# Kernel optimization log

Hardware: AMD Instinct MI355X
Metric: run time of the kernel (lower is better)

Reference implementation:

```python
import jax, jax.numpy as jnp
import numpy as np


def log_g(x):
    # log of g(x) = relu(x)+0.5 for x>=0, sigmoid(x) for x<0 (continuous minGRU activation)
    return jnp.where(x >= 0, jnp.log(jax.nn.relu(x) + 0.5), -jax.nn.softplus(-x))


def parallel_scan_log(log_coeffs, log_values):
    # log_coeffs: [B,T,H], log_values: [B,T+1,H]
    a_star = jnp.pad(jnp.cumsum(log_coeffs, axis=1), ((0, 0), (1, 0), (0, 0)))  # [B,T+1,H]
    log_h = a_star + jax.lax.cumlogsumexp(log_values - a_star, axis=1)
    return jnp.exp(log_h)  # [B,T+1,H]


def setup_inputs() -> dict:
    key = jax.random.key(0)
    B, T, D, H = 8, 4096, 1024, 1024
    k1, k2, k3, k4, k5, k6 = jax.random.split(key, 6)
    scale = 1.0 / np.sqrt(D)
    return {
        "x": jax.random.normal(k1, (B, T, D), dtype=jnp.float32),
        "h_0": jax.random.uniform(k2, (B, 1, H), dtype=jnp.float32),
        "W_z": jax.random.uniform(k3, (H, D), minval=-scale, maxval=scale, dtype=jnp.float32),
        "b_z": jax.random.uniform(k4, (H,), minval=-scale, maxval=scale, dtype=jnp.float32),
        "W_h": jax.random.uniform(k5, (H, D), minval=-scale, maxval=scale, dtype=jnp.float32),
        "b_h": jax.random.uniform(k6, (H,), minval=-scale, maxval=scale, dtype=jnp.float32),
    }


def reference(x, h_0, W_z, b_z, W_h, b_h):
    # k = linear_z(x)
    k = jnp.einsum('btd,hd->bth', x, W_z) + b_z                 # [B,T,H]
    log_z = -jax.nn.softplus(-k)                                # log sigmoid(k)
    log_coeffs = -jax.nn.softplus(k)                            # log (1 - sigmoid(k))
    log_h_0 = log_g(h_0)                                        # [B,1,H]
    log_tilde_h = log_g(jnp.einsum('btd,hd->bth', x, W_h) + b_h)  # [B,T,H]
    log_values = jnp.concatenate([log_h_0, log_z + log_tilde_h], axis=1)  # [B,T+1,H]
    h = parallel_scan_log(log_coeffs, log_values)               # [B,T+1,H]
    return h
```

## Files before the change

### kernel.cpp

```cpp
#include <hip/hip_runtime.h>
#include <stdint.h>

#define B_ 8
#define T_ 4096
#define D_ 1024
#define H_ 1024
#define M_ (B_*T_)
#define K_ D_
#define N_ H_
#define TC 64
#define NC (T_/TC)

typedef short short8 __attribute__((ext_vector_type(8)));
typedef float f32x4 __attribute__((ext_vector_type(4)));
typedef unsigned short ushort8v __attribute__((ext_vector_type(8)));

__device__ __forceinline__ float bf2f(unsigned short u) {
    union { unsigned int i; float f; } x; x.i = ((unsigned int)u) << 16; return x.f;
}
__device__ __forceinline__ unsigned short f2bf(float f) {
    union { float f; unsigned int i; } x; x.f = f;
    unsigned int u = x.i;
    unsigned int r = u + 0x7fffu + ((u >> 16) & 1u);
    return (unsigned short)(r >> 16);
}
__device__ __forceinline__ void gld_lds16(const unsigned short* g, unsigned short* l) {
    __builtin_amdgcn_global_load_lds(
        (const __attribute__((address_space(1))) void*)(const void*)g,
        (__attribute__((address_space(3))) void*)(void*)l, 16, 0, 0);
}
__device__ __forceinline__ float gfun(float x) {
    return x >= 0.f ? x + 0.5f : 1.f / (1.f + __expf(-x));
}

__global__ void cvt_kernel(const float* __restrict__ src, unsigned short* __restrict__ dst, int n4) {
    int i = blockIdx.x * blockDim.x + threadIdx.x;
    const int stride = gridDim.x * blockDim.x;
    for (; i < n4; i += stride) {
        float4 v = ((const float4*)src)[i];
        ushort4 o;
        o.x = f2bf(v.x); o.y = f2bf(v.y); o.z = f2bf(v.z); o.w = f2bf(v.w);
        ((ushort4*)dst)[i] = o;
    }
}

__global__ __launch_bounds__(256) void gemm_kernel(
    const unsigned short* __restrict__ Xb,
    const unsigned short* __restrict__ Wzb,
    const unsigned short* __restrict__ Whb,
    const float* __restrict__ bz, const float* __restrict__ bh,
    unsigned short* __restrict__ KzOut, unsigned short* __restrict__ KhOut)
{
    __shared__ __align__(16) unsigned short lds_a[128 * 32];
    __shared__ __align__(16) unsigned short lds_b[128 * 32];

    const int bm = blockIdx.x;
    const int bn = blockIdx.y;
    const int mat = blockIdx.z;
    const unsigned short* Wb = mat ? Whb : Wzb;
    const float* bias = mat ? bh : bz;
    unsigned short* Out = mat ? KhOut : KzOut;

    const int tid = threadIdx.x;
    const int w = tid >> 6, lane = tid & 63;
    const int wm = w >> 1, wn = w & 1;

    f32x4 acc[4][4];
#pragma unroll
    for (int i = 0; i < 4; i++)
#pragma unroll
        for (int j = 0; j < 4; j++) acc[i][j] = (f32x4){0.f, 0.f, 0.f, 0.f};

    const int kcs = ((lane & 3) ^ ((lane >> 3) & 3)) * 8;
    const int r0 = (w * 2 + 0) * 16 + (lane >> 2);
    const int r1 = (w * 2 + 1) * 16 + (lane >> 2);
    const unsigned short* gA0 = Xb + (size_t)(bm * 128 + r0) * K_ + kcs;
    const unsigned short* gA1 = Xb + (size_t)(bm * 128 + r1) * K_ + kcs;
    const unsigned short* gB0 = Wb + (size_t)(bn * 128 + r0) * K_ + kcs;
    const unsigned short* gB1 = Wb + (size_t)(bn * 128 + r1) * K_ + kcs;
    unsigned short* la0 = &lds_a[(w * 2 + 0) * 512];
    unsigned short* la1 = &lds_a[(w * 2 + 1) * 512];
    unsigned short* lb0 = &lds_b[(w * 2 + 0) * 512];
    unsigned short* lb1 = &lds_b[(w * 2 + 1) * 512];

    const int sw = ((lane >> 4) ^ ((lane >> 1) & 3)) * 8;
    const unsigned short* ra = &lds_a[(wm * 64 + (lane & 15)) * 32 + sw];
    const unsigned short* rb = &lds_b[(wn * 64 + (lane & 15)) * 32 + sw];

    for (int k0 = 0; k0 < K_; k0 += 32) {
        __syncthreads();
        gld_lds16(gA0 + k0, la0);
        gld_lds16(gA1 + k0, la1);
        gld_lds16(gB0 + k0, lb0);
        gld_lds16(gB1 + k0, lb1);
        __syncthreads();

        short8 af[4], bfr[4];
#pragma unroll
        for (int im = 0; im < 4; im++) af[im] = *(const short8*)(ra + im * 16 * 32);
#pragma unroll
        for (int in = 0; in < 4; in++) bfr[in] = *(const short8*)(rb + in * 16 * 32);
#pragma unroll
        for (int im = 0; im < 4; im++)
#pragma unroll
            for (int in = 0; in < 4; in++)
                acc[im][in] = __builtin_amdgcn_mfma_f32_16x16x32_bf16(af[im], bfr[in], acc[im][in], 0, 0, 0);
    }

#pragma unroll
    for (int in = 0; in < 4; in++) {
        const int n = bn * 128 + wn * 64 + in * 16 + (lane & 15);
        const float bb = bias[n];
#pragma unroll
        for (int im = 0; im < 4; im++) {
            const int mq = bm * 32 + wm * 16 + im * 4 + (lane >> 4);
            ushort4 o;
            o.x = f2bf(acc[im][in][0] + bb);
            o.y = f2bf(acc[im][in][1] + bb);
            o.z = f2bf(acc[im][in][2] + bb);
            o.w = f2bf(acc[im][in][3] + bb);
            *(ushort4*)(Out + ((size_t)mq * N_ + n) * 4) = o;
        }
    }
}


__global__ __launch_bounds__(256) void scanA_kernel(const unsigned short* __restrict__ Kz,
                                                    const unsigned short* __restrict__ Kh,
                                                    float* __restrict__ Fc, float* __restrict__ Vc)
{
    const int c = blockIdx.x, b = blockIdx.y;
    const int hb = threadIdx.x * 4;
    float F[4] = {1.f, 1.f, 1.f, 1.f}, V[4] = {0.f, 0.f, 0.f, 0.f};
    size_t base = ((size_t)(b * 1024 + c * (TC / 4)) * N_ + hb) * 4;
    for (int q = 0; q < TC / 4; q++) {
        ushort8v z0 = *(const ushort8v*)(Kz + base);
        ushort8v z1 = *(const ushort8v*)(Kz + base + 8);
        ushort8v h0v = *(const ushort8v*)(Kh + base);
        ushort8v h1v = *(const ushort8v*)(Kh + base + 8);
        base += (size_t)N_ * 4;
#pragma unroll
        for (int r = 0; r < 4; r++) {
            float kzf[4] = {bf2f(z0[r]), bf2f(z0[4 + r]), bf2f(z1[r]), bf2f(z1[4 + r])};
            float khf[4] = {bf2f(h0v[r]), bf2f(h0v[4 + r]), bf2f(h1v[r]), bf2f(h1v[4 + r])};
#pragma unroll
            for (int j = 0; j < 4; j++) {
                float f = 1.f / (1.f + __expf(kzf[j]));
                float v = (1.f - f) * gfun(khf[j]);
                V[j] = f * V[j] + v;
                F[j] *= f;
            }
        }
    }
    size_t o = ((size_t)(b * NC + c)) * H_ + hb;
    *(float4*)(Fc + o) = make_float4(F[0], F[1], F[2], F[3]);
    *(float4*)(Vc + o) = make_float4(V[0], V[1], V[2], V[3]);
}

__global__ __launch_bounds__(256) void scanB_kernel(const float* __restrict__ h0,
                                                    const float* __restrict__ Fc,
                                                    const float* __restrict__ Vc,
                                                    float* __restrict__ Carry,
                                                    float* __restrict__ Out)
{
    const int b = blockIdx.x;
    const int h = threadIdx.x * 4;
    float cy[4];
#pragma unroll
    for (int j = 0; j < 4; j++) cy[j] = gfun(h0[(size_t)b * H_ + h + j]);
    *(float4*)(Out + (size_t)b * (T_ + 1) * H_ + h) = make_float4(cy[0], cy[1], cy[2], cy[3]);
    for (int c = 0; c < NC; c++) {
        size_t o = ((size_t)(b * NC + c)) * H_ + h;
        *(float4*)(Carry + o) = make_float4(cy[0], cy[1], cy[2], cy[3]);
        float4 F4 = *(const float4*)(Fc + o);
        float4 V4 = *(const float4*)(Vc + o);
        cy[0] = F4.x * cy[0] + V4.x;
        cy[1] = F4.y * cy[1] + V4.y;
        cy[2] = F4.z * cy[2] + V4.z;
        cy[3] = F4.w * cy[3] + V4.w;
    }
}

__global__ __launch_bounds__(256) void scanC_kernel(const unsigned short* __restrict__ Kz,
                                                    const unsigned short* __restrict__ Kh,
                                                    const float* __restrict__ Carry,
                                                    float* __restrict__ Out)
{
    const int c = blockIdx.x, b = blockIdx.y;
    const int hb = threadIdx.x * 4;
    float cy[4];
    {
        float4 c4 = *(const float4*)(Carry + ((size_t)(b * NC + c)) * H_ + hb);
        cy[0] = c4.x; cy[1] = c4.y; cy[2] = c4.z; cy[3] = c4.w;
    }
    size_t base = ((size_t)(b * 1024 + c * (TC / 4)) * N_ + hb) * 4;
    size_t ob = ((size_t)(b * (T_ + 1) + c * TC + 1)) * H_ + hb;
    for (int q = 0; q < TC / 4; q++) {
        ushort8v z0 = *(const ushort8v*)(Kz + base);
        ushort8v z1 = *(const ushort8v*)(Kz + base + 8);
        ushort8v h0v = *(const ushort8v*)(Kh + base);
        ushort8v h1v = *(const ushort8v*)(Kh + base + 8);
        base += (size_t)N_ * 4;
#pragma unroll
        for (int r = 0; r < 4; r++) {
            float kzf[4] = {bf2f(z0[r]), bf2f(z0[4 + r]), bf2f(z1[r]), bf2f(z1[4 + r])};
            float khf[4] = {bf2f(h0v[r]), bf2f(h0v[4 + r]), bf2f(h1v[r]), bf2f(h1v[4 + r])};
#pragma unroll
            for (int j = 0; j < 4; j++) {
                float f = 1.f / (1.f + __expf(kzf[j]));
                float v = (1.f - f) * gfun(khf[j]);
                cy[j] = f * cy[j] + v;
            }
            *(float4*)(Out + ob) = make_float4(cy[0], cy[1], cy[2], cy[3]);
            ob += H_;
        }
    }
}

extern "C" void kernel_launch(void* const* d_in, const int* in_sizes, int n_in,
                              void* d_out, int out_size, void* d_ws, size_t ws_size,
                              hipStream_t stream)
{
    const float* x  = (const float*)d_in[0];
    const float* h0 = (const float*)d_in[1];
    const float* Wz = (const float*)d_in[2];
    const float* bz = (const float*)d_in[3];
    const float* Wh = (const float*)d_in[4];
    const float* bh = (const float*)d_in[5];
    float* out = (float*)d_out;

    char* ws = (char*)d_ws;
    unsigned short* xb  = (unsigned short*)ws; ws += (size_t)M_ * K_ * 2;
    unsigned short* wzb = (unsigned short*)ws; ws += (size_t)N_ * K_ * 2;
    unsigned short* whb = (unsigned short*)ws; ws += (size_t)N_ * K_ * 2;
    unsigned short* kz  = (unsigned short*)ws; ws += (size_t)M_ * N_ * 2;
    unsigned short* kh  = (unsigned short*)ws; ws += (size_t)M_ * N_ * 2;
    float* Fc    = (float*)ws; ws += (size_t)B_ * NC * H_ * 4;
    float* Vc    = (float*)ws; ws += (size_t)B_ * NC * H_ * 4;
    float* Carry = (float*)ws; ws += (size_t)B_ * NC * H_ * 4;

    cvt_kernel<<<2048, 256, 0, stream>>>(x, xb, M_ * K_ / 4);
    cvt_kernel<<<256, 256, 0, stream>>>(Wz, wzb, N_ * K_ / 4);
    cvt_kernel<<<256, 256, 0, stream>>>(Wh, whb, N_ * K_ / 4);

    dim3 gg(M_ / 128, N_ / 128, 2);
    gemm_kernel<<<gg, 256, 0, stream>>>(xb, wzb, whb, bz, bh, kz, kh);

    scanA_kernel<<<dim3(NC, B_), 256, 0, stream>>>(kz, kh, Fc, Vc);
    scanB_kernel<<<B_, 256, 0, stream>>>(h0, Fc, Vc, Carry, out);
    scanC_kernel<<<dim3(NC, B_), 256, 0, stream>>>(kz, kh, Carry, out);
}
```

Measured before the change: 506.3 us.

## Merge conversion launches, swizzle GEMM block order, and halve scan chunk size

Combines the three fp32-to-bf16 conversion launches into one kernel that dispatches on block index, removing two launch overheads. Remaps the GEMM grid to a 1D linear index grouped so that 8 M-tiles share all N-tiles and both weight matrices, improving L2 reuse of X rows. Halves the scan chunk length so the chunked scan passes launch twice as many blocks for more parallelism, at the cost of a longer sequential carry pass in scanB and more chunk-summary traffic.

```diff
diff --git a/kernel.cpp b/kernel.cpp
--- a/kernel.cpp
+++ b/kernel.cpp
@@ -8,7 +8,7 @@
 #define M_ (B_*T_)
 #define K_ D_
 #define N_ H_
-#define TC 64
+#define TC 32
 #define NC (T_/TC)
 
 typedef short short8 __attribute__((ext_vector_type(8)));
@@ -33,14 +33,22 @@
     return x >= 0.f ? x + 0.5f : 1.f / (1.f + __expf(-x));
 }
 
-__global__ void cvt_kernel(const float* __restrict__ src, unsigned short* __restrict__ dst, int n4) {
-    int i = blockIdx.x * blockDim.x + threadIdx.x;
-    const int stride = gridDim.x * blockDim.x;
-    for (; i < n4; i += stride) {
-        float4 v = ((const float4*)src)[i];
+__global__ void cvt3_kernel(const float* __restrict__ x, const float* __restrict__ wz,
+                            const float* __restrict__ wh,
+                            unsigned short* __restrict__ xb, unsigned short* __restrict__ wzb,
+                            unsigned short* __restrict__ whb)
+{
+    const float* s; unsigned short* d; int n4; int bid;
+    if (blockIdx.x < 2048)      { s = x;  d = xb;  n4 = M_ * K_ / 4; bid = blockIdx.x;        }
+    else if (blockIdx.x < 2080) { s = wz; d = wzb; n4 = N_ * K_ / 4; bid = blockIdx.x - 2048; }
+    else                        { s = wh; d = whb; n4 = N_ * K_ / 4; bid = blockIdx.x - 2080; }
+    const int nblocks = (blockIdx.x < 2048) ? 2048 : 32;
+    const int stride = nblocks * 256;
+    for (int i = bid * 256 + threadIdx.x; i < n4; i += stride) {
+        float4 v = ((const float4*)s)[i];
         ushort4 o;
         o.x = f2bf(v.x); o.y = f2bf(v.y); o.z = f2bf(v.z); o.w = f2bf(v.w);
-        ((ushort4*)dst)[i] = o;
+        ((ushort4*)d)[i] = o;
     }
 }
 
@@ -54,9 +62,13 @@
     __shared__ __align__(16) unsigned short lds_a[128 * 32];
     __shared__ __align__(16) unsigned short lds_b[128 * 32];
 
-    const int bm = blockIdx.x;
-    const int bn = blockIdx.y;
-    const int mat = blockIdx.z;
+    const int lin = blockIdx.x;
+    const int g   = lin >> 7;
+    const int wi  = lin & 127;
+    const int bm  = (g << 3) | (wi >> 4);
+    const int bn  = (wi >> 1) & 7;
+    const int mat = wi & 1;
+
     const unsigned short* Wb = mat ? Whb : Wzb;
     const float* bias = mat ? bh : bz;
     unsigned short* Out = mat ? KhOut : KzOut;
@@ -132,7 +144,7 @@
     const int c = blockIdx.x, b = blockIdx.y;
     const int hb = threadIdx.x * 4;
     float F[4] = {1.f, 1.f, 1.f, 1.f}, V[4] = {0.f, 0.f, 0.f, 0.f};
-    size_t base = ((size_t)(b * 1024 + c * (TC / 4)) * N_ + hb) * 4;
+    size_t base = ((size_t)(b * (T_ / 4) + c * (TC / 4)) * N_ + hb) * 4;
     for (int q = 0; q < TC / 4; q++) {
         ushort8v z0 = *(const ushort8v*)(Kz + base);
         ushort8v z1 = *(const ushort8v*)(Kz + base + 8);
@@ -193,7 +205,7 @@
         float4 c4 = *(const float4*)(Carry + ((size_t)(b * NC + c)) * H_ + hb);
         cy[0] = c4.x; cy[1] = c4.y; cy[2] = c4.z; cy[3] = c4.w;
     }
-    size_t base = ((size_t)(b * 1024 + c * (TC / 4)) * N_ + hb) * 4;
+    size_t base = ((size_t)(b * (T_ / 4) + c * (TC / 4)) * N_ + hb) * 4;
     size_t ob = ((size_t)(b * (T_ + 1) + c * TC + 1)) * H_ + hb;
     for (int q = 0; q < TC / 4; q++) {
         ushort8v z0 = *(const ushort8v*)(Kz + base);
@@ -239,12 +251,9 @@
     float* Vc    = (float*)ws; ws += (size_t)B_ * NC * H_ * 4;
     float* Carry = (float*)ws; ws += (size_t)B_ * NC * H_ * 4;
 
-    cvt_kernel<<<2048, 256, 0, stream>>>(x, xb, M_ * K_ / 4);
-    cvt_kernel<<<256, 256, 0, stream>>>(Wz, wzb, N_ * K_ / 4);
-    cvt_kernel<<<256, 256, 0, stream>>>(Wh, whb, N_ * K_ / 4);
-
-    dim3 gg(M_ / 128, N_ / 128, 2);
-    gemm_kernel<<<gg, 256, 0, stream>>>(xb, wzb, whb, bz, bh, kz, kh);
+    cvt3_kernel<<<2112, 256, 0, stream>>>(x, Wz, Wh, xb, wzb, whb);
+
+    gemm_kernel<<<4096, 256, 0, stream>>>(xb, wzb, whb, bz, bh, kz, kh);
 
     scanA_kernel<<<dim3(NC, B_), 256, 0, stream>>>(kz, kh, Fc, Vc);
     scanB_kernel<<<B_, 256, 0, stream>>>(h0, Fc, Vc, Carry, out);
```

Result: no change. 509.4 us (+0.6%).
